# Optimization experiments

Hardware: AMD Instinct MI355X
Metric: run time of the kernel (lower is better)

The kernel has to match this reference:

```python
import jax, jax.numpy as jnp
import numpy as np

B, T, D = 2, 2048, 1024
H, G, K = 16, 4, 64          # num_heads, num_kv_heads, head_dim
R = H // G                   # GQA repeat factor
F = 4096                     # mlp_dim
EPS = 1e-6


def rms_norm(x, scale, eps=EPS):
    var = jnp.mean(x.astype(jnp.float32) ** 2, axis=-1, keepdims=True)
    normed = x * jax.lax.rsqrt(var + eps)
    return (scale * normed).astype(x.dtype)


def apply_rope(x_BTHK, sin_BTK, cos_BTK):
    half = x_BTHK.shape[-1] // 2
    x1, x2 = x_BTHK[..., :half], x_BTHK[..., half:]
    s = sin_BTK[:, :, None, :]
    c = cos_BTK[:, :, None, :]
    return jnp.concatenate([x1 * c - x2 * s, x2 * c + x1 * s], axis=-1).astype(x_BTHK.dtype)


def setup_inputs() -> dict:
    key = jax.random.key(0)
    ks = jax.random.split(key, 12)
    hidden_BTD = jax.random.normal(ks[0], (B, T, D), jnp.float32)
    # rope tables: realistic sin/cos of position*inv_freq
    inv_freq = 1.0 / (10000.0 ** (jnp.arange(K // 2, dtype=jnp.float32) / (K // 2)))
    ang = jnp.arange(T, dtype=jnp.float32)[:, None] * inv_freq[None, :]  # [T, K/2]
    sin_BTK = jnp.broadcast_to(jnp.sin(ang)[None], (B, T, K // 2))
    cos_BTK = jnp.broadcast_to(jnp.cos(ang)[None], (B, T, K // 2))
    mask = jnp.broadcast_to(jnp.tril(jnp.ones((T, T), bool))[None], (B, T, T))
    sc = 1.0 / np.sqrt(D)
    scf = 1.0 / np.sqrt(F)
    return {
        "hidden_BTD": hidden_BTD, "sin_BTK": sin_BTK, "cos_BTK": cos_BTK, "mask": mask,
        "ln1_scale": jnp.ones((D,), jnp.float32),
        "ln2_scale": jnp.ones((D,), jnp.float32),
        "qn_scale": jnp.ones((K,), jnp.float32),
        "kn_scale": jnp.ones((K,), jnp.float32),
        "q_w": jax.random.normal(ks[1], (D, H * K), jnp.float32) * sc,
        "k_w": jax.random.normal(ks[2], (D, G * K), jnp.float32) * sc,
        "v_w": jax.random.normal(ks[3], (D, G * K), jnp.float32) * sc,
        "o_w": jax.random.normal(ks[4], (H * K, D), jnp.float32) * sc,
        "gate_w": jax.random.normal(ks[5], (D, F), jnp.float32) * sc,
        "up_w": jax.random.normal(ks[6], (D, F), jnp.float32) * sc,
        "down_w": jax.random.normal(ks[7], (F, D), jnp.float32) * scf,
    }


def reference(hidden_BTD, sin_BTK, cos_BTK, mask, ln1_scale, ln2_scale,
              qn_scale, kn_scale, q_w, k_w, v_w, o_w, gate_w, up_w, down_w):
    x = rms_norm(hidden_BTD, ln1_scale)
    q = rms_norm((x @ q_w).reshape(B, T, H, K), qn_scale)
    k = rms_norm((x @ k_w).reshape(B, T, G, K), kn_scale)
    v = (x @ v_w).reshape(B, T, G, K)
    q = apply_rope(q, sin_BTK, cos_BTK)
    k = apply_rope(k, sin_BTK, cos_BTK)
    q_BTGRK = q.reshape(B, T, G, R, K)
    scale = K ** (-0.5)
    logits = jnp.einsum('BTGRK,BSGK->BTSGR', q_BTGRK, k) * scale
    neg = float(jnp.finfo(logits.dtype).min)
    logits = jnp.where(mask[:, :, :, None, None], logits, neg)
    weights = jax.nn.softmax(logits.astype(jnp.float32), axis=2).astype(logits.dtype)
    attn = jnp.einsum('BTSGR,BSGK->BTGRK', weights, v).reshape(B, T, H * K)
    hidden_BTD = hidden_BTD + attn @ o_w
    y = rms_norm(hidden_BTD, ln2_scale)
    ff = (jax.nn.silu(y @ gate_w) * (y @ up_w)) @ down_w
    return hidden_BTD + ff
```

## Files before the change

kernel.cpp:

```cpp
#include <hip/hip_runtime.h>
#include <hip/hip_bf16.h>

#define EPSF 1e-6f
constexpr int Bsz  = 2;
constexpr int Tseq = 2048;
constexpr int Dmod = 1024;
constexpr int Hh   = 16;
constexpr int Gg   = 4;
constexpr int Ff   = 4096;
constexpr int Mrows = Bsz * Tseq;

typedef __attribute__((ext_vector_type(8))) short bf16x8;
typedef __attribute__((ext_vector_type(4))) float f32x4;
typedef unsigned short u16;

__device__ inline u16 f2bf(float x) {
    union { float f; unsigned u; } v; v.f = x;
    unsigned r = v.u + 0x7fff + ((v.u >> 16) & 1);
    return (u16)(r >> 16);
}
__device__ inline float bf2f(u16 h) {
    union { unsigned u; float f; } v; v.u = ((unsigned)h) << 16; return v.f;
}

__device__ __forceinline__ void async_copy16(const u16* g, u16* l) {
    __builtin_amdgcn_global_load_lds(
        (const __attribute__((address_space(1))) void*)g,
        (__attribute__((address_space(3))) void*)l, 16, 0, 0);
}


__global__ __launch_bounds__(256) void wprep_all_kernel(
    const float* __restrict__ q_w, const float* __restrict__ k_w,
    const float* __restrict__ v_w, const float* __restrict__ o_w,
    const float* __restrict__ gate_w, const float* __restrict__ up_w,
    const float* __restrict__ down_w,
    u16* __restrict__ QKVT, u16* __restrict__ OTh, u16* __restrict__ OTl,
    u16* __restrict__ GTh, u16* __restrict__ UTh, u16* __restrict__ DTh)
{
    const int bx = blockIdx.x;
    const float* W; u16* Th; u16* Tl = nullptr;
    int N, Kd, ntile, ktile, drow;
    if (bx < 1024) {
        W = q_w; N = 1024; Kd = 1024; ntile = bx & 31; ktile = bx >> 5;
        Th = QKVT; drow = ntile * 32;
    } else if (bx < 1280) {
        const int i = bx - 1024;
        W = k_w; N = 256; Kd = 1024; ntile = i & 7; ktile = i >> 3;
        Th = QKVT; drow = 1024 + ntile * 32;
    } else if (bx < 1536) {
        const int i = bx - 1280;
        W = v_w; N = 256; Kd = 1024; ntile = i & 7; ktile = i >> 3;
        Th = QKVT; drow = 1280 + ntile * 32;
    } else if (bx < 2560) {
        const int i = bx - 1536;
        W = o_w; N = 1024; Kd = 1024; ntile = i & 31; ktile = i >> 5;
        Th = OTh; Tl = OTl; drow = ntile * 32;
    } else if (bx < 6656) {
        const int i = bx - 2560;
        W = gate_w; N = 4096; Kd = 1024; ntile = i & 127; ktile = i >> 7;
        Th = GTh; drow = ntile * 32;
    } else if (bx < 10752) {
        const int i = bx - 6656;
        W = up_w; N = 4096; Kd = 1024; ntile = i & 127; ktile = i >> 7;
        Th = UTh; drow = ntile * 32;
    } else {
        const int i = bx - 10752;
        W = down_w; N = 1024; Kd = 4096; ntile = i & 31; ktile = i >> 5;
        Th = DTh; drow = ntile * 32;
    }
    const int n0 = ntile * 32, k0 = ktile * 32;

    __shared__ float tile[32][33];
    const int r = threadIdx.x >> 3, c4 = (threadIdx.x & 7) * 4;
    const float4 v = *reinterpret_cast<const float4*>(&W[(size_t)(k0 + r) * N + n0 + c4]);
    tile[r][c4 + 0] = v.x; tile[r][c4 + 1] = v.y;
    tile[r][c4 + 2] = v.z; tile[r][c4 + 3] = v.w;
    __syncthreads();
    const int nl = threadIdx.x >> 3, kq = (threadIdx.x & 7) * 4;
    float x0 = tile[kq + 0][nl], x1 = tile[kq + 1][nl];
    float x2 = tile[kq + 2][nl], x3 = tile[kq + 3][nl];
    ushort4 h;
    h.x = f2bf(x0); h.y = f2bf(x1); h.z = f2bf(x2); h.w = f2bf(x3);
    *reinterpret_cast<ushort4*>(&Th[(size_t)(drow + nl) * Kd + k0 + kq]) = h;
    if (Tl) {
        ushort4 l;
        l.x = f2bf(x0 - bf2f(h.x)); l.y = f2bf(x1 - bf2f(h.y));
        l.z = f2bf(x2 - bf2f(h.z)); l.w = f2bf(x3 - bf2f(h.w));
        *reinterpret_cast<ushort4*>(&Tl[(size_t)(drow + nl) * Kd + k0 + kq]) = l;
    }
}

template <int LO>
__global__ __launch_bounds__(256) void rmsnorm_split_kernel(
    const float* __restrict__ x, const float* __restrict__ scale,
    u16* __restrict__ oh, u16* __restrict__ ol)
{
    const int row = blockIdx.x;
    const int tid = threadIdx.x;
    const float4 v = reinterpret_cast<const float4*>(x + (size_t)row * Dmod)[tid];
    float ss = v.x * v.x + v.y * v.y + v.z * v.z + v.w * v.w;
    #pragma unroll
    for (int off = 32; off; off >>= 1) ss += __shfl_xor(ss, off, 64);
    __shared__ float part[4];
    if ((tid & 63) == 0) part[tid >> 6] = ss;
    __syncthreads();
    const float tot = part[0] + part[1] + part[2] + part[3];
    const float rstd = rsqrtf(tot * (1.0f / Dmod) + EPSF);
    const float4 sc = reinterpret_cast<const float4*>(scale)[tid];
    float o0 = v.x * rstd * sc.x, o1 = v.y * rstd * sc.y;
    float o2 = v.z * rstd * sc.z, o3 = v.w * rstd * sc.w;
    ushort4 h;
    h.x = f2bf(o0); h.y = f2bf(o1); h.z = f2bf(o2); h.w = f2bf(o3);
    *reinterpret_cast<ushort4*>(&oh[(size_t)row * Dmod + tid * 4]) = h;
    if (LO) {
        ushort4 l;
        l.x = f2bf(o0 - bf2f(h.x)); l.y = f2bf(o1 - bf2f(h.y));
        l.z = f2bf(o2 - bf2f(h.z)); l.w = f2bf(o3 - bf2f(h.w));
        *reinterpret_cast<ushort4*>(&ol[(size_t)row * Dmod + tid * 4]) = l;
    }
}

template <int ASPLIT, int BSPLIT, int RES>
__global__ __launch_bounds__(256, 2) void mfma_gemm_kernel(
    const u16* __restrict__ Ah, const u16* __restrict__ Al,
    const u16* __restrict__ Bh, const u16* __restrict__ Bl,
    const float* __restrict__ res, float* __restrict__ C,
    int M, int N, int Kd)
{
    __shared__ u16 As_h[128 * 32];
    __shared__ u16 As_l[128 * 32];
    __shared__ u16 Bs_h[128 * 32];
    __shared__ u16 Bs_l[128 * 32];

    const int tid = threadIdx.x;
    const int lane = tid & 63, wave = tid >> 6;
    const int wm = (wave >> 1) * 64, wn = (wave & 1) * 64;
    const int m0 = blockIdx.y * 128, n0 = blockIdx.x * 128;
    const int fm = lane & 15, quad = lane >> 4;
    const int fsw = (fm >> 1) & 3;
    const int fcol = ((quad ^ fsw) * 8);

    f32x4 acc[4][4];
    #pragma unroll
    for (int i = 0; i < 4; ++i)
        #pragma unroll
        for (int j = 0; j < 4; ++j) acc[i][j] = (f32x4){0.f, 0.f, 0.f, 0.f};

    const int lrow = lane >> 2;
    const int lchunk = lane & 3;
    const int schunk = lchunk ^ ((lrow >> 1) & 3);

    for (int k0 = 0; k0 < Kd; k0 += 32) {
        __syncthreads();
        #pragma unroll
        for (int p = 0; p < 2; ++p) {
            const int row = wave * 32 + p * 16 + lrow;
            const size_t ga = (size_t)(m0 + row) * Kd + k0 + schunk * 8;
            const size_t gb = (size_t)(n0 + row) * Kd + k0 + schunk * 8;
            const int ls = row * 32 + lchunk * 8;
            async_copy16(&Ah[ga], &As_h[ls]);
            if (ASPLIT) async_copy16(&Al[ga], &As_l[ls]);
            async_copy16(&Bh[gb], &Bs_h[ls]);
            if (BSPLIT) async_copy16(&Bl[gb], &Bs_l[ls]);
        }
        __syncthreads();

        bf16x8 ah[4], al[4], bh[4], bl[4];
        #pragma unroll
        for (int t = 0; t < 4; ++t) {
            const int ra = (wm + t * 16 + fm) * 32 + fcol;
            const int rb = (wn + t * 16 + fm) * 32 + fcol;
            ah[t] = *reinterpret_cast<const bf16x8*>(&As_h[ra]);
            bh[t] = *reinterpret_cast<const bf16x8*>(&Bs_h[rb]);
            if (ASPLIT) al[t] = *reinterpret_cast<const bf16x8*>(&As_l[ra]);
            if (BSPLIT) bl[t] = *reinterpret_cast<const bf16x8*>(&Bs_l[rb]);
        }
        #pragma unroll
        for (int mt = 0; mt < 4; ++mt)
            #pragma unroll
            for (int nt = 0; nt < 4; ++nt) {
                acc[mt][nt] = __builtin_amdgcn_mfma_f32_16x16x32_bf16(
                    ah[mt], bh[nt], acc[mt][nt], 0, 0, 0);
                if (BSPLIT)
                    acc[mt][nt] = __builtin_amdgcn_mfma_f32_16x16x32_bf16(
                        ah[mt], bl[nt], acc[mt][nt], 0, 0, 0);
                if (ASPLIT)
                    acc[mt][nt] = __builtin_amdgcn_mfma_f32_16x16x32_bf16(
                        al[mt], bh[nt], acc[mt][nt], 0, 0, 0);
            }
    }

    const int cr = (lane >> 4) * 4, cn = lane & 15;
    #pragma unroll
    for (int mt = 0; mt < 4; ++mt)
        #pragma unroll
        for (int nt = 0; nt < 4; ++nt)
            #pragma unroll
            for (int r = 0; r < 4; ++r) {
                const int gm = m0 + wm + mt * 16 + cr + r;
                const int gn = n0 + wn + nt * 16 + cn;
                float v = acc[mt][nt][r];
                if (RES) v += res[(size_t)gm * N + gn];
                C[(size_t)gm * N + gn] = v;
            }
}

__global__ __launch_bounds__(256, 2) void qkv_fused_kernel(
    const u16* __restrict__ Ah, const u16* __restrict__ Bh,
    const float* __restrict__ qn, const float* __restrict__ kn,
    const float* __restrict__ sinp, const float* __restrict__ cosp,
    u16* __restrict__ Qbh, u16* __restrict__ Qbl,
    u16* __restrict__ Kbh, u16* __restrict__ Kbl,
    u16* __restrict__ Vth, u16* __restrict__ Vtl)
{
    __shared__ u16 As_h[128 * 32];
    __shared__ u16 Bs_h[128 * 32];

    const int Kd = 1024;
    const int tid = threadIdx.x;
    const int lane = tid & 63, wave = tid >> 6;
    const int wm = (wave >> 1) * 64, wn = (wave & 1) * 64;
    const int m0 = blockIdx.y * 128, n0 = blockIdx.x * 128;
    const int fm = lane & 15, quad = lane >> 4;
    const int fsw = (fm >> 1) & 3;
    const int fcol = ((quad ^ fsw) * 8);

    f32x4 acc[4][4];
    #pragma unroll
    for (int i = 0; i < 4; ++i)
        #pragma unroll
        for (int j = 0; j < 4; ++j) acc[i][j] = (f32x4){0.f, 0.f, 0.f, 0.f};

    const int lrow = lane >> 2;
    const int lchunk = lane & 3;
    const int schunk = lchunk ^ ((lrow >> 1) & 3);

    for (int k0 = 0; k0 < Kd; k0 += 32) {
        __syncthreads();
        #pragma unroll
        for (int p = 0; p < 2; ++p) {
            const int row = wave * 32 + p * 16 + lrow;
            const size_t ga = (size_t)(m0 + row) * Kd + k0 + schunk * 8;
            const size_t gb = (size_t)(n0 + row) * Kd + k0 + schunk * 8;
            const int ls = row * 32 + lchunk * 8;
            async_copy16(&Ah[ga], &As_h[ls]);
            async_copy16(&Bh[gb], &Bs_h[ls]);
        }
        __syncthreads();

        bf16x8 ah[4], bh[4];
        #pragma unroll
        for (int t = 0; t < 4; ++t) {
            ah[t] = *reinterpret_cast<const bf16x8*>(&As_h[(wm + t * 16 + fm) * 32 + fcol]);
            bh[t] = *reinterpret_cast<const bf16x8*>(&Bs_h[(wn + t * 16 + fm) * 32 + fcol]);
        }
        #pragma unroll
        for (int mt = 0; mt < 4; ++mt)
            #pragma unroll
            for (int nt = 0; nt < 4; ++nt)
                acc[mt][nt] = __builtin_amdgcn_mfma_f32_16x16x32_bf16(
                    ah[mt], bh[nt], acc[mt][nt], 0, 0, 0);
    }

    const int gn0 = n0 + wn;
    const int l15 = lane & 15;

    if (gn0 < 1280) {
        const bool isQ = (gn0 < 1024);
        const float* nsc = isQ ? qn : kn;
        const float osc = isQ ? 0.125f : 1.0f;
        u16* __restrict__ oh = isQ ? Qbh : Kbh;
        u16* __restrict__ ol = isQ ? Qbl : Kbl;
        const int rowstride = isQ ? 1024 : 256;
        const int colbase = isQ ? gn0 : gn0 - 1024;
        float sc[4];
        #pragma unroll
        for (int nt = 0; nt < 4; ++nt) sc[nt] = nsc[nt * 16 + l15];

        #pragma unroll
        for (int mt = 0; mt < 4; ++mt)
            #pragma unroll
            for (int r = 0; r < 4; ++r) {
                const int bt = m0 + wm + mt * 16 + quad * 4 + r;
                float v[4];
                #pragma unroll
                for (int nt = 0; nt < 4; ++nt) v[nt] = acc[mt][nt][r];
                float ss = v[0] * v[0] + v[1] * v[1] + v[2] * v[2] + v[3] * v[3];
                #pragma unroll
                for (int off = 1; off < 16; off <<= 1)
                    ss += __shfl_xor(ss, off, 16);
                const float rstd = rsqrtf(ss * (1.0f / 64.0f) + EPSF);
                float nv[4];
                #pragma unroll
                for (int nt = 0; nt < 4; ++nt) nv[nt] = v[nt] * rstd * sc[nt];
                const float s0 = sinp[bt * 32 + l15];
                const float c0 = cosp[bt * 32 + l15];
                const float s1 = sinp[bt * 32 + 16 + l15];
                const float c1 = cosp[bt * 32 + 16 + l15];
                float o[4];
                o[0] = (nv[0] * c0 - nv[2] * s0) * osc;
                o[1] = (nv[1] * c1 - nv[3] * s1) * osc;
                o[2] = (nv[2] * c0 + nv[0] * s0) * osc;
                o[3] = (nv[3] * c1 + nv[1] * s1) * osc;
                #pragma unroll
                for (int nt = 0; nt < 4; ++nt) {
                    const size_t off = (size_t)bt * rowstride + colbase + nt * 16 + l15;
                    const u16 hi = f2bf(o[nt]);
                    oh[off] = hi;
                    ol[off] = f2bf(o[nt] - bf2f(hi));
                }
            }
    } else {
        const int g = (gn0 - 1280) >> 6;
        const int b = (m0 + wm) >> 11;
        const int tb = ((m0 + wm) & 2047) + quad * 4;
        #pragma unroll
        for (int mt = 0; mt < 4; ++mt)
            #pragma unroll
            for (int nt = 0; nt < 4; ++nt) {
                const float v0 = acc[mt][nt][0], v1 = acc[mt][nt][1];
                const float v2 = acc[mt][nt][2], v3 = acc[mt][nt][3];
                ushort4 hv, lv;
                hv.x = f2bf(v0); hv.y = f2bf(v1); hv.z = f2bf(v2); hv.w = f2bf(v3);
                lv.x = f2bf(v0 - bf2f(hv.x)); lv.y = f2bf(v1 - bf2f(hv.y));
                lv.z = f2bf(v2 - bf2f(hv.z)); lv.w = f2bf(v3 - bf2f(hv.w));
                const size_t off =
                    ((size_t)((b * 4 + g) * 64 + nt * 16 + l15)) * Tseq + tb + mt * 16;
                *reinterpret_cast<ushort4*>(&Vth[off]) = hv;
                *reinterpret_cast<ushort4*>(&Vtl[off]) = lv;
            }
    }
}

#define GU_PHASE_SYNC()                                       \
    __builtin_amdgcn_s_barrier();                             \
    asm volatile("s_waitcnt lgkmcnt(0)" ::: "memory");        \
    __builtin_amdgcn_sched_barrier(0)

#define GU_MFMA4(MBASE, AF)                                                      \
    _Pragma("unroll")                                                            \
    for (int mf = 0; mf < 4; ++mf) {                                             \
        accg[(MBASE) + mf][0] = __builtin_amdgcn_mfma_f32_16x16x32_bf16(         \
            AF[mf], bgf[0], accg[(MBASE) + mf][0], 0, 0, 0);                     \
        accu[(MBASE) + mf][0] = __builtin_amdgcn_mfma_f32_16x16x32_bf16(         \
            AF[mf], buf2[0], accu[(MBASE) + mf][0], 0, 0, 0);                    \
        accg[(MBASE) + mf][1] = __builtin_amdgcn_mfma_f32_16x16x32_bf16(         \
            AF[mf], bgf[1], accg[(MBASE) + mf][1], 0, 0, 0);                     \
        accu[(MBASE) + mf][1] = __builtin_amdgcn_mfma_f32_16x16x32_bf16(         \
            AF[mf], buf2[1], accu[(MBASE) + mf][1], 0, 0, 0);                    \
    }

__global__ __launch_bounds__(512, 2) void gateup8_kernel(
    const u16* __restrict__ Yh, const u16* __restrict__ Yl,
    const u16* __restrict__ Gw, const u16* __restrict__ Uw,
    u16* __restrict__ FF)
{
    constexpr int NK = 32;
    __shared__ u16 AsH[3][256 * 32];
    __shared__ u16 AsL[3][256 * 32];
    __shared__ u16 Gs[3][128 * 32];
    __shared__ u16 Us[3][128 * 32];

    const int tid  = threadIdx.x;
    const int lane = tid & 63;
    const int wave = tid >> 6;
    const int wave_m = wave >> 2;
    const int wave_n = wave & 3;

    const int wg  = blockIdx.x;
    const int xcd = wg & 7;
    const int idx = wg >> 3;
    const int ntile = xcd * 4 + (idx & 3);
    const int mtile = idx >> 2;
    const int m0 = mtile * 256, n0 = ntile * 128;

    const int fm = lane & 15, quad = lane >> 4;
    const int fsw = (fm >> 1) & 3;
    const int fcol = (quad ^ fsw) * 8;

    f32x4 accg[8][2], accu[8][2];
    #pragma unroll
    for (int i = 0; i < 8; ++i)
        #pragma unroll
        for (int j = 0; j < 2; ++j) {
            accg[i][j] = (f32x4){0.f, 0.f, 0.f, 0.f};
            accu[i][j] = (f32x4){0.f, 0.f, 0.f, 0.f};
        }

    const int srow = tid >> 2;
    const int schk = tid & 3;
    const int sw   = schk ^ ((srow >> 1) & 3);
    const u16* aSrc0 = &Yh[(size_t)(m0 + srow) * 1024 + sw * 8];
    const u16* aSrc1 = &Yh[(size_t)(m0 + srow + 128) * 1024 + sw * 8];
    const u16* lSrc0 = &Yl[(size_t)(m0 + srow) * 1024 + sw * 8];
    const u16* lSrc1 = &Yl[(size_t)(m0 + srow + 128) * 1024 + sw * 8];
    const u16* gSrc  = &Gw[(size_t)(n0 + srow) * 1024 + sw * 8];
    const u16* uSrc  = &Uw[(size_t)(n0 + srow) * 1024 + sw * 8];
    const int aDst0 = srow * 32 + schk * 8;
    const int aDst1 = aDst0 + 128 * 32;

#define STAGE_AH(T, BUF) do {                                  \
        async_copy16(aSrc0 + (T) * 32, &AsH[BUF][aDst0]);      \
        async_copy16(aSrc1 + (T) * 32, &AsH[BUF][aDst1]); } while (0)
#define STAGE_AL(T, BUF) do {                                  \
        async_copy16(lSrc0 + (T) * 32, &AsL[BUF][aDst0]);      \
        async_copy16(lSrc1 + (T) * 32, &AsL[BUF][aDst1]); } while (0)
#define STAGE_B(T, BUF) do {                                   \
        async_copy16(gSrc + (T) * 32, &Gs[BUF][aDst0]);        \
        async_copy16(uSrc + (T) * 32, &Us[BUF][aDst0]); } while (0)

    int raOff[8], rbOff[2];
    #pragma unroll
    for (int mf = 0; mf < 8; ++mf)
        raOff[mf] = (wave_m * 128 + mf * 16 + fm) * 32 + fcol;
    #pragma unroll
    for (int nf = 0; nf < 2; ++nf)
        rbOff[nf] = (wave_n * 32 + nf * 16 + fm) * 32 + fcol;

    STAGE_AH(0, 0); STAGE_AL(0, 0); STAGE_B(0, 0);
    STAGE_AH(1, 1); STAGE_AL(1, 1); STAGE_B(1, 1);
    asm volatile("s_waitcnt vmcnt(6)" ::: "memory");
    __builtin_amdgcn_s_barrier();

    int bcur = 0, bnxt = 2;
    #pragma unroll 1
    for (int t = 0; t < NK; ++t) {
        const bool pf = (t + 2 < NK);
        bf16x8 bgf[2], buf2[2];

        {
            #pragma unroll
            for (int nf = 0; nf < 2; ++nf) {
                bgf[nf]  = *reinterpret_cast<const bf16x8*>(&Gs[bcur][rbOff[nf]]);
                buf2[nf] = *reinterpret_cast<const bf16x8*>(&Us[bcur][rbOff[nf]]);
            }
            bf16x8 af[4];
            #pragma unroll
            for (int mf = 0; mf < 4; ++mf)
                af[mf] = *reinterpret_cast<const bf16x8*>(&AsH[bcur][raOff[mf]]);
            if (pf) STAGE_AH(t + 2, bnxt);
            GU_PHASE_SYNC();
            __builtin_amdgcn_s_setprio(1);
            GU_MFMA4(0, af);
            __builtin_amdgcn_s_setprio(0);
            __builtin_amdgcn_s_barrier();
        }
        {
            bf16x8 af[4];
            #pragma unroll
            for (int mf = 0; mf < 4; ++mf)
                af[mf] = *reinterpret_cast<const bf16x8*>(&AsH[bcur][raOff[mf + 4]]);
            if (pf) STAGE_AL(t + 2, bnxt);
            GU_PHASE_SYNC();
            __builtin_amdgcn_s_setprio(1);
            GU_MFMA4(4, af);
            __builtin_amdgcn_s_setprio(0);
            __builtin_amdgcn_s_barrier();
        }
        {
            bf16x8 af[4];
            #pragma unroll
            for (int mf = 0; mf < 4; ++mf)
                af[mf] = *reinterpret_cast<const bf16x8*>(&AsL[bcur][raOff[mf]]);
            if (pf) STAGE_B(t + 2, bnxt);
            GU_PHASE_SYNC();
            __builtin_amdgcn_s_setprio(1);
            GU_MFMA4(0, af);
            __builtin_amdgcn_s_setprio(0);
            __builtin_amdgcn_s_barrier();
        }
        {
            bf16x8 af[4];
            #pragma unroll
            for (int mf = 0; mf < 4; ++mf)
                af[mf] = *reinterpret_cast<const bf16x8*>(&AsL[bcur][raOff[mf + 4]]);
            GU_PHASE_SYNC();
            __builtin_amdgcn_s_setprio(1);
            GU_MFMA4(4, af);
            __builtin_amdgcn_s_setprio(0);
            if (t + 2 < NK) {
                asm volatile("s_waitcnt vmcnt(6)" ::: "memory");
            } else if (t + 1 < NK) {
                asm volatile("s_waitcnt vmcnt(0)" ::: "memory");
            }
            __builtin_amdgcn_s_barrier();
        }

        bcur = (bcur == 2) ? 0 : bcur + 1;
        bnxt = (bnxt == 2) ? 0 : bnxt + 1;
    }
#undef STAGE_AH
#undef STAGE_AL
#undef STAGE_B

    const int cr = quad * 4;
    #pragma unroll
    for (int mf = 0; mf < 8; ++mf)
        #pragma unroll
        for (int nf = 0; nf < 2; ++nf)
            #pragma unroll
            for (int r = 0; r < 4; ++r) {
                const int gm = m0 + wave_m * 128 + mf * 16 + cr + r;
                const int gn = n0 + wave_n * 32 + nf * 16 + fm;
                const float g = accg[mf][nf][r];
                const float ff = (g / (1.0f + __expf(-g))) * accu[mf][nf][r];
                FF[(size_t)gm * Ff + gn] = f2bf(ff);
            }
}

__global__ __launch_bounds__(256) void attn_mfma_kernel(
    const u16* __restrict__ Qh, const u16* __restrict__ Ql,
    const u16* __restrict__ Kh, const u16* __restrict__ Kl,
    const u16* __restrict__ Vth, const u16* __restrict__ Vtl,
    u16* __restrict__ AOh, u16* __restrict__ AOl)
{
    __shared__ u16 KsH[64 * 72];
    __shared__ u16 KsL[64 * 72];
    __shared__ u16 VsH[64 * 72];
    __shared__ u16 VsL[64 * 72];
    __shared__ u16 Ps[4][16 * 72];

    const int tid = threadIdx.x;
    const int wave = tid >> 6, lane = tid & 63;
    const int l15 = lane & 15, quad = lane >> 4;

    const int bg = blockIdx.x & 7;
    const int b = bg >> 2, g = bg & 3;
    const int win = 127 - (blockIdx.x >> 3);
    const int t0 = win * 16;
    const int h = g * 4 + wave;

    bf16x8 qh[2], ql[2];
    {
        const size_t qrow = (size_t)(b * Tseq + t0 + l15) * 1024 + h * 64;
        #pragma unroll
        for (int ks = 0; ks < 2; ++ks) {
            qh[ks] = *reinterpret_cast<const bf16x8*>(&Qh[qrow + ks * 32 + quad * 8]);
            ql[ks] = *reinterpret_cast<const bf16x8*>(&Ql[qrow + ks * 32 + quad * 8]);
        }
    }

    const int srow = tid >> 2;
    const int scol = (tid & 3) * 16;
    const size_t kgb = (size_t)(b * Tseq) * 256 + g * 64 + scol;
    const size_t vgb = (size_t)(bg * 64 + srow) * Tseq + scol;

    const int nit = t0 / 64 + 1;

    uint4 ck0, ck1, cl0, cl1, cv0, cv1, cw0, cw1;
    {
        const size_t ka = kgb + (size_t)srow * 256;
        ck0 = *reinterpret_cast<const uint4*>(&Kh[ka]);
        ck1 = *reinterpret_cast<const uint4*>(&Kh[ka + 8]);
        cl0 = *reinterpret_cast<const uint4*>(&Kl[ka]);
        cl1 = *reinterpret_cast<const uint4*>(&Kl[ka + 8]);
        cv0 = *reinterpret_cast<const uint4*>(&Vth[vgb]);
        cv1 = *reinterpret_cast<const uint4*>(&Vth[vgb + 8]);
        cw0 = *reinterpret_cast<const uint4*>(&Vtl[vgb]);
        cw1 = *reinterpret_cast<const uint4*>(&Vtl[vgb + 8]);
    }

    f32x4 oacc[4];
    #pragma unroll
    for (int nt = 0; nt < 4; ++nt) oacc[nt] = (f32x4){0.f, 0.f, 0.f, 0.f};
    float m_r[4], l_r[4];
    #pragma unroll
    for (int r = 0; r < 4; ++r) { m_r[r] = -1e30f; l_r[r] = 0.0f; }

    u16* psw = &Ps[wave][0];
    const int lb = srow * 72 + scol;

    for (int it = 0; it < nit; ++it) {
        const int s0 = it * 64;
        const bool diag = (it == nit - 1);

        __syncthreads();
        *reinterpret_cast<uint4*>(&KsH[lb])     = ck0;
        *reinterpret_cast<uint4*>(&KsH[lb + 8]) = ck1;
        *reinterpret_cast<uint4*>(&KsL[lb])     = cl0;
        *reinterpret_cast<uint4*>(&KsL[lb + 8]) = cl1;
        *reinterpret_cast<uint4*>(&VsH[lb])     = cv0;
        *reinterpret_cast<uint4*>(&VsH[lb + 8]) = cv1;
        *reinterpret_cast<uint4*>(&VsL[lb])     = cw0;
        *reinterpret_cast<uint4*>(&VsL[lb + 8]) = cw1;
        if (it + 1 < nit) {
            const size_t ka = kgb + (size_t)(s0 + 64 + srow) * 256;
            ck0 = *reinterpret_cast<const uint4*>(&Kh[ka]);
            ck1 = *reinterpret_cast<const uint4*>(&Kh[ka + 8]);
            cl0 = *reinterpret_cast<const uint4*>(&Kl[ka]);
            cl1 = *reinterpret_cast<const uint4*>(&Kl[ka + 8]);
            const size_t va = vgb + s0 + 64;
            cv0 = *reinterpret_cast<const uint4*>(&Vth[va]);
            cv1 = *reinterpret_cast<const uint4*>(&Vth[va + 8]);
            cw0 = *reinterpret_cast<const uint4*>(&Vtl[va]);
            cw1 = *reinterpret_cast<const uint4*>(&Vtl[va + 8]);
        }
        __syncthreads();

        f32x4 sacc[4];
        #pragma unroll
        for (int nt = 0; nt < 4; ++nt) sacc[nt] = (f32x4){0.f, 0.f, 0.f, 0.f};

        #pragma unroll
        for (int ks = 0; ks < 2; ++ks) {
            bf16x8 kfh[4], kfl[4];
            #pragma unroll
            for (int nt = 0; nt < 4; ++nt) {
                const int a = (nt * 16 + l15) * 72 + ks * 32 + quad * 8;
                kfh[nt] = *reinterpret_cast<const bf16x8*>(&KsH[a]);
                kfl[nt] = *reinterpret_cast<const bf16x8*>(&KsL[a]);
            }
            #pragma unroll
            for (int nt = 0; nt < 4; ++nt) {
                sacc[nt] = __builtin_amdgcn_mfma_f32_16x16x32_bf16(qh[ks], kfh[nt], sacc[nt], 0, 0, 0);
                sacc[nt] = __builtin_amdgcn_mfma_f32_16x16x32_bf16(ql[ks], kfh[nt], sacc[nt], 0, 0, 0);
                sacc[nt] = __builtin_amdgcn_mfma_f32_16x16x32_bf16(qh[ks], kfl[nt], sacc[nt], 0, 0, 0);
            }
        }

        if (diag) {
            #pragma unroll
            for (int nt = 0; nt < 4; ++nt) {
                const int sg = s0 + nt * 16 + l15;
                #pragma unroll
                for (int r = 0; r < 4; ++r)
                    if (sg > t0 + quad * 4 + r) sacc[nt][r] = -1e30f;
            }
        }

        #pragma unroll
        for (int r = 0; r < 4; ++r) {
            float mx = fmaxf(fmaxf(sacc[0][r], sacc[1][r]),
                             fmaxf(sacc[2][r], sacc[3][r]));
            #pragma unroll
            for (int off = 1; off < 16; off <<= 1)
                mx = fmaxf(mx, __shfl_xor(mx, off, 16));
            const float mnew = fmaxf(m_r[r], mx);
            const float alpha = __expf(m_r[r] - mnew);
            m_r[r] = mnew;

            float rs = 0.0f;
            #pragma unroll
            for (int nt = 0; nt < 4; ++nt) {
                const float p = __expf(sacc[nt][r] - mnew);
                sacc[nt][r] = p;
                rs += p;
            }
            #pragma unroll
            for (int off = 1; off < 16; off <<= 1)
                rs += __shfl_xor(rs, off, 16);
            l_r[r] = l_r[r] * alpha + rs;
            #pragma unroll
            for (int nt = 0; nt < 4; ++nt) oacc[nt][r] *= alpha;
            #pragma unroll
            for (int nt = 0; nt < 4; ++nt)
                psw[(quad * 4 + r) * 72 + nt * 16 + l15] = f2bf(sacc[nt][r]);
        }

        #pragma unroll
        for (int ks = 0; ks < 2; ++ks) {
            const bf16x8 pa = *reinterpret_cast<const bf16x8*>(
                &psw[l15 * 72 + ks * 32 + quad * 8]);
            bf16x8 vfh[4], vfl[4];
            #pragma unroll
            for (int nt = 0; nt < 4; ++nt) {
                const int a = (nt * 16 + l15) * 72 + ks * 32 + quad * 8;
                vfh[nt] = *reinterpret_cast<const bf16x8*>(&VsH[a]);
                vfl[nt] = *reinterpret_cast<const bf16x8*>(&VsL[a]);
            }
            #pragma unroll
            for (int nt = 0; nt < 4; ++nt) {
                oacc[nt] = __builtin_amdgcn_mfma_f32_16x16x32_bf16(pa, vfh[nt], oacc[nt], 0, 0, 0);
                oacc[nt] = __builtin_amdgcn_mfma_f32_16x16x32_bf16(pa, vfl[nt], oacc[nt], 0, 0, 0);
            }
        }
    }

    #pragma unroll
    for (int r = 0; r < 4; ++r) {
        const float inv = 1.0f / l_r[r];
        const size_t orow = (size_t)(b * Tseq + t0 + quad * 4 + r) * 1024 + h * 64;
        #pragma unroll
        for (int nt = 0; nt < 4; ++nt) {
            const float o = oacc[nt][r] * inv;
            const u16 hi = f2bf(o);
            AOh[orow + nt * 16 + l15] = hi;
            AOl[orow + nt * 16 + l15] = f2bf(o - bf2f(hi));
        }
    }
}

extern "C" void kernel_launch(void* const* d_in, const int* in_sizes, int n_in,
                              void* d_out, int out_size, void* d_ws,
                              size_t ws_size, hipStream_t stream)
{
    const float* hidden = (const float*)d_in[0];
    const float* sinp   = (const float*)d_in[1];
    const float* cosp   = (const float*)d_in[2];
    const float* ln1    = (const float*)d_in[4];
    const float* ln2    = (const float*)d_in[5];
    const float* qn     = (const float*)d_in[6];
    const float* kn     = (const float*)d_in[7];
    const float* q_w    = (const float*)d_in[8];
    const float* k_w    = (const float*)d_in[9];
    const float* v_w    = (const float*)d_in[10];
    const float* o_w    = (const float*)d_in[11];
    const float* gate_w = (const float*)d_in[12];
    const float* up_w   = (const float*)d_in[13];
    const float* down_w = (const float*)d_in[14];
    float* out = (float*)d_out;

    char* base = (char*)d_ws;
    u16*   OTh  = (u16*)(base);
    u16*   OTl  = (u16*)(base + 2097152);
    u16*   GTh  = (u16*)(base + 4194304);
    u16*   UTh  = (u16*)(base + 12582912);
    u16*   DTh  = (u16*)(base + 20971520);
    u16*   QKVT = (u16*)(base + 29360128);
    u16*   Xh   = (u16*)(base + 32505856);
    u16*   Qbh  = (u16*)(base + 40894464);
    u16*   Qbl  = (u16*)(base + 49283072);
    u16*   Kbh  = (u16*)(base + 57671680);
    u16*   Kbl  = (u16*)(base + 59768832);
    u16*   Vth  = (u16*)(base + 61865984);
    u16*   Vtl  = (u16*)(base + 63963136);
    u16*   AOh  = (u16*)(base + 66060288);
    u16*   AOl  = (u16*)(base + 74448896);
    u16*   FFh  = (u16*)(base + 82837504);

    float* H2 = (float*)Qbh;
    u16*   Yh = Kbh;
    u16*   Yl = AOh;

    wprep_all_kernel<<<14848, 256, 0, stream>>>(
        q_w, k_w, v_w, o_w, gate_w, up_w, down_w,
        QKVT, OTh, OTl, GTh, UTh, DTh);

    rmsnorm_split_kernel<0><<<Mrows, 256, 0, stream>>>(hidden, ln1, Xh, nullptr);

    qkv_fused_kernel<<<dim3(12, 32), 256, 0, stream>>>(
        Xh, QKVT, qn, kn, sinp, cosp, Qbh, Qbl, Kbh, Kbl, Vth, Vtl);

    attn_mfma_kernel<<<Bsz * Gg * (Tseq / 16), 256, 0, stream>>>(
        Qbh, Qbl, Kbh, Kbl, Vth, Vtl, AOh, AOl);

    mfma_gemm_kernel<1, 1, 1><<<dim3(8, 32), 256, 0, stream>>>(
        AOh, AOl, OTh, OTl, hidden, H2, Mrows, Dmod, 1024);

    rmsnorm_split_kernel<1><<<Mrows, 256, 0, stream>>>(H2, ln2, Yh, Yl);

    gateup8_kernel<<<512, 512, 0, stream>>>(Yh, Yl, GTh, UTh, FFh);

    mfma_gemm_kernel<0, 0, 1><<<dim3(8, 32), 256, 0, stream>>>(
        FFh, nullptr, DTh, nullptr, H2, out, Mrows, Dmod, 4096);
}
```

Baseline: 521.5 us.

## Switch gate/up GEMM to 32x32x16 MFMA with two-phase pipeline and manual unroll

Rewrites the gate/up FFN kernel to use 32x32x16 bf16 MFMA tiles instead of 16x16x32, which cuts LDS fragment reads per FLOP and the number of MFMA issues. The four per-iteration phases become two (hi and lo activation halves), so there are fewer barriers per K-step. The triple-buffer rotation is unrolled by three with constant buffer indices, and the epilogue is remapped to the 32x32 accumulator layout. This adds register pressure and a different LDS swizzle access pattern, and prefetches are grouped more densely in the second phase.

```diff
diff --git a/kernel.cpp b/kernel.cpp
--- a/kernel.cpp
+++ b/kernel.cpp
@@ -12,6 +12,7 @@
 
 typedef __attribute__((ext_vector_type(8))) short bf16x8;
 typedef __attribute__((ext_vector_type(4))) float f32x4;
+typedef __attribute__((ext_vector_type(16))) float f32x16;
 typedef unsigned short u16;
 
 __device__ inline u16 f2bf(float x) {
@@ -338,20 +339,7 @@
     asm volatile("s_waitcnt lgkmcnt(0)" ::: "memory");        \
     __builtin_amdgcn_sched_barrier(0)
 
-#define GU_MFMA4(MBASE, AF)                                                      \
-    _Pragma("unroll")                                                            \
-    for (int mf = 0; mf < 4; ++mf) {                                             \
-        accg[(MBASE) + mf][0] = __builtin_amdgcn_mfma_f32_16x16x32_bf16(         \
-            AF[mf], bgf[0], accg[(MBASE) + mf][0], 0, 0, 0);                     \
-        accu[(MBASE) + mf][0] = __builtin_amdgcn_mfma_f32_16x16x32_bf16(         \
-            AF[mf], buf2[0], accu[(MBASE) + mf][0], 0, 0, 0);                    \
-        accg[(MBASE) + mf][1] = __builtin_amdgcn_mfma_f32_16x16x32_bf16(         \
-            AF[mf], bgf[1], accg[(MBASE) + mf][1], 0, 0, 0);                     \
-        accu[(MBASE) + mf][1] = __builtin_amdgcn_mfma_f32_16x16x32_bf16(         \
-            AF[mf], buf2[1], accu[(MBASE) + mf][1], 0, 0, 0);                    \
-    }
-
-__global__ __launch_bounds__(512, 2) void gateup8_kernel(
+__global__ __launch_bounds__(512, 2) void gateup32_kernel(
     const u16* __restrict__ Yh, const u16* __restrict__ Yl,
     const u16* __restrict__ Gw, const u16* __restrict__ Uw,
     u16* __restrict__ FF)
@@ -375,18 +363,15 @@
     const int mtile = idx >> 2;
     const int m0 = mtile * 256, n0 = ntile * 128;
 
-    const int fm = lane & 15, quad = lane >> 4;
-    const int fsw = (fm >> 1) & 3;
-    const int fcol = (quad ^ fsw) * 8;
-
-    f32x4 accg[8][2], accu[8][2];
-    #pragma unroll
-    for (int i = 0; i < 8; ++i)
-        #pragma unroll
-        for (int j = 0; j < 2; ++j) {
-            accg[i][j] = (f32x4){0.f, 0.f, 0.f, 0.f};
-            accu[i][j] = (f32x4){0.f, 0.f, 0.f, 0.f};
-        }
+    const int l31 = lane & 31;
+    const int khi = lane >> 5;
+
+    f32x16 accg[4], accu[4];
+    #pragma unroll
+    for (int i = 0; i < 4; ++i) {
+        accg[i] = (f32x16)(0.f);
+        accu[i] = (f32x16)(0.f);
+    }
 
     const int srow = tid >> 2;
     const int schk = tid & 3;
@@ -410,103 +395,110 @@
         async_copy16(gSrc + (T) * 32, &Gs[BUF][aDst0]);        \
         async_copy16(uSrc + (T) * 32, &Us[BUF][aDst0]); } while (0)
 
-    int raOff[8], rbOff[2];
-    #pragma unroll
-    for (int mf = 0; mf < 8; ++mf)
-        raOff[mf] = (wave_m * 128 + mf * 16 + fm) * 32 + fcol;
-    #pragma unroll
-    for (int nf = 0; nf < 2; ++nf)
-        rbOff[nf] = (wave_n * 32 + nf * 16 + fm) * 32 + fcol;
+    int aOff[4][2], bOff[2];
+    #pragma unroll
+    for (int mf = 0; mf < 4; ++mf)
+        #pragma unroll
+        for (int h = 0; h < 2; ++h) {
+            const int ra = wave_m * 128 + mf * 32 + l31;
+            aOff[mf][h] = ra * 32 + (((2 * h + khi) ^ ((ra >> 1) & 3)) * 8);
+        }
+    #pragma unroll
+    for (int h = 0; h < 2; ++h) {
+        const int rb = wave_n * 32 + l31;
+        bOff[h] = rb * 32 + (((2 * h + khi) ^ ((rb >> 1) & 3)) * 8);
+    }
+
+#define GU_STEP(BC, BN, T, PF, GATE) do {                                       \
+    bf16x8 bg[2], bu[2];                                                        \
+    {                                                    \
+        bf16x8 ah[4][2];                                                        \
+        _Pragma("unroll")                                                       \
+        for (int h = 0; h < 2; ++h) {                                           \
+            bg[h] = *reinterpret_cast<const bf16x8*>(&Gs[BC][bOff[h]]);         \
+            bu[h] = *reinterpret_cast<const bf16x8*>(&Us[BC][bOff[h]]);         \
+        }                                                                       \
+        _Pragma("unroll")                                                       \
+        for (int mf = 0; mf < 4; ++mf)                                          \
+            _Pragma("unroll")                                                   \
+            for (int h = 0; h < 2; ++h)                                         \
+                ah[mf][h] = *reinterpret_cast<const bf16x8*>(                   \
+                    &AsH[BC][aOff[mf][h]]);                                     \
+        if (PF) STAGE_AH((T) + 2, BN);                                          \
+        GU_PHASE_SYNC();                                                        \
+        __builtin_amdgcn_s_setprio(1);                                          \
+        _Pragma("unroll")                                                       \
+        for (int mf = 0; mf < 4; ++mf)                                          \
+            _Pragma("unroll")                                                   \
+            for (int h = 0; h < 2; ++h) {                                       \
+                accg[mf] = __builtin_amdgcn_mfma_f32_32x32x16_bf16(             \
+                    ah[mf][h], bg[h], accg[mf], 0, 0, 0);                       \
+                accu[mf] = __builtin_amdgcn_mfma_f32_32x32x16_bf16(             \
+                    ah[mf][h], bu[h], accu[mf], 0, 0, 0);                       \
+            }                                                                   \
+        __builtin_amdgcn_s_setprio(0);                                          \
+        __builtin_amdgcn_s_barrier();                                           \
+    }                                                                           \
+    {                                                    \
+        bf16x8 al[4][2];                                                        \
+        _Pragma("unroll")                                                       \
+        for (int mf = 0; mf < 4; ++mf)                                          \
+            _Pragma("unroll")                                                   \
+            for (int h = 0; h < 2; ++h)                                         \
+                al[mf][h] = *reinterpret_cast<const bf16x8*>(                   \
+                    &AsL[BC][aOff[mf][h]]);                                     \
+        if (PF) { STAGE_AL((T) + 2, BN); STAGE_B((T) + 2, BN); }                \
+        GU_PHASE_SYNC();                                                        \
+        __builtin_amdgcn_s_setprio(1);                                          \
+        _Pragma("unroll")                                                       \
+        for (int mf = 0; mf < 4; ++mf)                                          \
+            _Pragma("unroll")                                                   \
+            for (int h = 0; h < 2; ++h) {                                       \
+                accg[mf] = __builtin_amdgcn_mfma_f32_32x32x16_bf16(             \
+                    al[mf][h], bg[h], accg[mf], 0, 0, 0);                       \
+                accu[mf] = __builtin_amdgcn_mfma_f32_32x32x16_bf16(             \
+                    al[mf][h], bu[h], accu[mf], 0, 0, 0);                       \
+            }                                                                   \
+        __builtin_amdgcn_s_setprio(0);                                          \
+        if ((GATE) == 6) {                                                      \
+            asm volatile("s_waitcnt vmcnt(6)" ::: "memory");                    \
+        } else if ((GATE) == 0) {                                               \
+            asm volatile("s_waitcnt vmcnt(0)" ::: "memory");                    \
+        }                                                                       \
+        __builtin_amdgcn_s_barrier();                                           \
+    }                                                                           \
+} while (0)
 
     STAGE_AH(0, 0); STAGE_AL(0, 0); STAGE_B(0, 0);
     STAGE_AH(1, 1); STAGE_AL(1, 1); STAGE_B(1, 1);
     asm volatile("s_waitcnt vmcnt(6)" ::: "memory");
     __builtin_amdgcn_s_barrier();
 
-    int bcur = 0, bnxt = 2;
     #pragma unroll 1
-    for (int t = 0; t < NK; ++t) {
-        const bool pf = (t + 2 < NK);
-        bf16x8 bgf[2], buf2[2];
-
-        {
-            #pragma unroll
-            for (int nf = 0; nf < 2; ++nf) {
-                bgf[nf]  = *reinterpret_cast<const bf16x8*>(&Gs[bcur][rbOff[nf]]);
-                buf2[nf] = *reinterpret_cast<const bf16x8*>(&Us[bcur][rbOff[nf]]);
-            }
-            bf16x8 af[4];
-            #pragma unroll
-            for (int mf = 0; mf < 4; ++mf)
-                af[mf] = *reinterpret_cast<const bf16x8*>(&AsH[bcur][raOff[mf]]);
-            if (pf) STAGE_AH(t + 2, bnxt);
-            GU_PHASE_SYNC();
-            __builtin_amdgcn_s_setprio(1);
-            GU_MFMA4(0, af);
-            __builtin_amdgcn_s_setprio(0);
-            __builtin_amdgcn_s_barrier();
-        }
-        {
-            bf16x8 af[4];
-            #pragma unroll
-            for (int mf = 0; mf < 4; ++mf)
-                af[mf] = *reinterpret_cast<const bf16x8*>(&AsH[bcur][raOff[mf + 4]]);
-            if (pf) STAGE_AL(t + 2, bnxt);
-            GU_PHASE_SYNC();
-            __builtin_amdgcn_s_setprio(1);
-            GU_MFMA4(4, af);
-            __builtin_amdgcn_s_setprio(0);
-            __builtin_amdgcn_s_barrier();
-        }
-        {
-            bf16x8 af[4];
-            #pragma unroll
-            for (int mf = 0; mf < 4; ++mf)
-                af[mf] = *reinterpret_cast<const bf16x8*>(&AsL[bcur][raOff[mf]]);
-            if (pf) STAGE_B(t + 2, bnxt);
-            GU_PHASE_SYNC();
-            __builtin_amdgcn_s_setprio(1);
-            GU_MFMA4(0, af);
-            __builtin_amdgcn_s_setprio(0);
-            __builtin_amdgcn_s_barrier();
-        }
-        {
-            bf16x8 af[4];
-            #pragma unroll
-            for (int mf = 0; mf < 4; ++mf)
-                af[mf] = *reinterpret_cast<const bf16x8*>(&AsL[bcur][raOff[mf + 4]]);
-            GU_PHASE_SYNC();
-            __builtin_amdgcn_s_setprio(1);
-            GU_MFMA4(4, af);
-            __builtin_amdgcn_s_setprio(0);
-            if (t + 2 < NK) {
-                asm volatile("s_waitcnt vmcnt(6)" ::: "memory");
-            } else if (t + 1 < NK) {
-                asm volatile("s_waitcnt vmcnt(0)" ::: "memory");
-            }
-            __builtin_amdgcn_s_barrier();
-        }
-
-        bcur = (bcur == 2) ? 0 : bcur + 1;
-        bnxt = (bnxt == 2) ? 0 : bnxt + 1;
-    }
+    for (int t3 = 0; t3 < NK - 2; t3 += 3) {
+        GU_STEP(0, 2, t3 + 0, true, 6);
+        GU_STEP(1, 0, t3 + 1, true, 6);
+        GU_STEP(2, 1, t3 + 2, true, 6);
+    }
+    GU_STEP(0, 2, 30, false, 0);
+    GU_STEP(1, 0, 31, false, -1);
+
+#undef GU_STEP
 #undef STAGE_AH
 #undef STAGE_AL
 #undef STAGE_B
 
-    const int cr = quad * 4;
-    #pragma unroll
-    for (int mf = 0; mf < 8; ++mf)
-        #pragma unroll
-        for (int nf = 0; nf < 2; ++nf)
-            #pragma unroll
-            for (int r = 0; r < 4; ++r) {
-                const int gm = m0 + wave_m * 128 + mf * 16 + cr + r;
-                const int gn = n0 + wave_n * 32 + nf * 16 + fm;
-                const float g = accg[mf][nf][r];
-                const float ff = (g / (1.0f + __expf(-g))) * accu[mf][nf][r];
-                FF[(size_t)gm * Ff + gn] = f2bf(ff);
-            }
+    #pragma unroll
+    for (int mf = 0; mf < 4; ++mf)
+        #pragma unroll
+        for (int reg = 0; reg < 16; ++reg) {
+            const int crow = (reg & 3) + 8 * (reg >> 2) + 4 * khi;
+            const int gm = m0 + wave_m * 128 + mf * 32 + crow;
+            const int gn = n0 + wave_n * 32 + l31;
+            const float g = accg[mf][reg];
+            const float ff = (g / (1.0f + __expf(-g))) * accu[mf][reg];
+            FF[(size_t)gm * Ff + gn] = f2bf(ff);
+        }
 }
 
 __global__ __launch_bounds__(256) void attn_mfma_kernel(
@@ -750,7 +742,7 @@
 
     rmsnorm_split_kernel<1><<<Mrows, 256, 0, stream>>>(H2, ln2, Yh, Yl);
 
-    gateup8_kernel<<<512, 512, 0, stream>>>(Yh, Yl, GTh, UTh, FFh);
+    gateup32_kernel<<<512, 512, 0, stream>>>(Yh, Yl, GTh, UTh, FFh);
 
     mfma_gemm_kernel<0, 0, 1><<<dim3(8, 32), 256, 0, stream>>>(
         FFh, nullptr, DTh, nullptr, H2, out, Mrows, Dmod, 4096);
```

Result: slower. 534.3 us (+2.5%).

## Triple-buffer async loads in output GEMMs with explicit vmcnt gating

Applied to the files above, without the earlier changes.

Replaces the single-buffered GEMM used for the output projection and down projection with a three-stage software pipeline. Global-to-LDS async copies are issued two k-steps ahead and gated by explicit vmcnt waits, with raised wave priority around the MFMA block. The aim is to hide load latency and drop one barrier per k-step. It triples LDS use per block, which may lower occupancy for the split-precision variant, and it fixes K at compile time.

```diff
diff --git a/kernel.cpp b/kernel.cpp
--- a/kernel.cpp
+++ b/kernel.cpp
@@ -121,17 +121,21 @@
     }
 }
 
-template <int ASPLIT, int BSPLIT, int RES>
-__global__ __launch_bounds__(256, 2) void mfma_gemm_kernel(
+template <int NKT, int ASPLIT, int BSPLIT, int RES>
+__global__ __launch_bounds__(256, 2) void mfma_gemm_pipe(
     const u16* __restrict__ Ah, const u16* __restrict__ Al,
     const u16* __restrict__ Bh, const u16* __restrict__ Bl,
     const float* __restrict__ res, float* __restrict__ C,
-    int M, int N, int Kd)
+    int M, int N)
 {
-    __shared__ u16 As_h[128 * 32];
-    __shared__ u16 As_l[128 * 32];
-    __shared__ u16 Bs_h[128 * 32];
-    __shared__ u16 Bs_l[128 * 32];
+    constexpr int Kd = NKT * 32;
+    constexpr int NI = 4 + 4 * ASPLIT * 0 + 2 * ASPLIT + 2 * BSPLIT;
+    static_assert((NKT - 2) % 3 == 0, "main loop unroll-3");
+
+    __shared__ u16 AsH[3][128 * 32];
+    __shared__ u16 BsH[3][128 * 32];
+    __shared__ u16 AsL[ASPLIT ? 3 : 1][128 * 32];
+    __shared__ u16 BsL[BSPLIT ? 3 : 1][128 * 32];
 
     const int tid = threadIdx.x;
     const int lane = tid & 63, wave = tid >> 6;
@@ -139,7 +143,7 @@
     const int m0 = blockIdx.y * 128, n0 = blockIdx.x * 128;
     const int fm = lane & 15, quad = lane >> 4;
     const int fsw = (fm >> 1) & 3;
-    const int fcol = ((quad ^ fsw) * 8);
+    const int fcol = (quad ^ fsw) * 8;
 
     f32x4 acc[4][4];
     #pragma unroll
@@ -147,49 +151,97 @@
         #pragma unroll
         for (int j = 0; j < 4; ++j) acc[i][j] = (f32x4){0.f, 0.f, 0.f, 0.f};
 
-    const int lrow = lane >> 2;
-    const int lchunk = lane & 3;
-    const int schunk = lchunk ^ ((lrow >> 1) & 3);
-
-    for (int k0 = 0; k0 < Kd; k0 += 32) {
-        __syncthreads();
-        #pragma unroll
-        for (int p = 0; p < 2; ++p) {
-            const int row = wave * 32 + p * 16 + lrow;
-            const size_t ga = (size_t)(m0 + row) * Kd + k0 + schunk * 8;
-            const size_t gb = (size_t)(n0 + row) * Kd + k0 + schunk * 8;
-            const int ls = row * 32 + lchunk * 8;
-            async_copy16(&Ah[ga], &As_h[ls]);
-            if (ASPLIT) async_copy16(&Al[ga], &As_l[ls]);
-            async_copy16(&Bh[gb], &Bs_h[ls]);
-            if (BSPLIT) async_copy16(&Bl[gb], &Bs_l[ls]);
-        }
-        __syncthreads();
-
-        bf16x8 ah[4], al[4], bh[4], bl[4];
-        #pragma unroll
-        for (int t = 0; t < 4; ++t) {
-            const int ra = (wm + t * 16 + fm) * 32 + fcol;
-            const int rb = (wn + t * 16 + fm) * 32 + fcol;
-            ah[t] = *reinterpret_cast<const bf16x8*>(&As_h[ra]);
-            bh[t] = *reinterpret_cast<const bf16x8*>(&Bs_h[rb]);
-            if (ASPLIT) al[t] = *reinterpret_cast<const bf16x8*>(&As_l[ra]);
-            if (BSPLIT) bl[t] = *reinterpret_cast<const bf16x8*>(&Bs_l[rb]);
-        }
-        #pragma unroll
-        for (int mt = 0; mt < 4; ++mt)
-            #pragma unroll
-            for (int nt = 0; nt < 4; ++nt) {
-                acc[mt][nt] = __builtin_amdgcn_mfma_f32_16x16x32_bf16(
-                    ah[mt], bh[nt], acc[mt][nt], 0, 0, 0);
-                if (BSPLIT)
-                    acc[mt][nt] = __builtin_amdgcn_mfma_f32_16x16x32_bf16(
-                        ah[mt], bl[nt], acc[mt][nt], 0, 0, 0);
-                if (ASPLIT)
-                    acc[mt][nt] = __builtin_amdgcn_mfma_f32_16x16x32_bf16(
-                        al[mt], bh[nt], acc[mt][nt], 0, 0, 0);
-            }
-    }
+    const int srow = tid >> 2;
+    const int schk = tid & 3;
+    const int sw   = schk ^ ((srow >> 1) & 3);
+    const u16* aS0 = &Ah[(size_t)(m0 + srow) * Kd + sw * 8];
+    const u16* aS1 = &Ah[(size_t)(m0 + srow + 64) * Kd + sw * 8];
+    const u16* bS0 = &Bh[(size_t)(n0 + srow) * Kd + sw * 8];
+    const u16* bS1 = &Bh[(size_t)(n0 + srow + 64) * Kd + sw * 8];
+    const u16* alS0 = ASPLIT ? &Al[(size_t)(m0 + srow) * Kd + sw * 8] : nullptr;
+    const u16* alS1 = ASPLIT ? &Al[(size_t)(m0 + srow + 64) * Kd + sw * 8] : nullptr;
+    const u16* blS0 = BSPLIT ? &Bl[(size_t)(n0 + srow) * Kd + sw * 8] : nullptr;
+    const u16* blS1 = BSPLIT ? &Bl[(size_t)(n0 + srow + 64) * Kd + sw * 8] : nullptr;
+    const int dst0 = srow * 32 + schk * 8;
+    const int dst1 = dst0 + 64 * 32;
+
+#define PSTAGE(T, BUF) do {                                                  \
+        async_copy16(aS0 + (T) * 32, &AsH[BUF][dst0]);                       \
+        async_copy16(aS1 + (T) * 32, &AsH[BUF][dst1]);                       \
+        if (ASPLIT) {                                                        \
+            async_copy16(alS0 + (T) * 32, &AsL[BUF][dst0]);                  \
+            async_copy16(alS1 + (T) * 32, &AsL[BUF][dst1]);                  \
+        }                                                                    \
+        async_copy16(bS0 + (T) * 32, &BsH[BUF][dst0]);                       \
+        async_copy16(bS1 + (T) * 32, &BsH[BUF][dst1]);                       \
+        if (BSPLIT) {                                                        \
+            async_copy16(blS0 + (T) * 32, &BsL[BUF][dst0]);                  \
+            async_copy16(blS1 + (T) * 32, &BsL[BUF][dst1]);                  \
+        }                                                                    \
+    } while (0)
+
+#define PGATE(GATE) do {                                                     \
+        if ((GATE) == 1) {                                                   \
+            if constexpr (NI == 4)                                           \
+                asm volatile("s_waitcnt vmcnt(4)" ::: "memory");             \
+            else                                                             \
+                asm volatile("s_waitcnt vmcnt(8)" ::: "memory");             \
+        } else if ((GATE) == 0) {                                            \
+            asm volatile("s_waitcnt vmcnt(0)" ::: "memory");                 \
+        }                                                                    \
+    } while (0)
+
+#define PSTEP(BC, BN, T, PF, GATE) do {                                      \
+    bf16x8 ah[4], bh[4], al[4], bl[4];                                       \
+    _Pragma("unroll")                                                        \
+    for (int t = 0; t < 4; ++t) {                                            \
+        const int ra = (wm + t * 16 + fm) * 32 + fcol;                       \
+        const int rb = (wn + t * 16 + fm) * 32 + fcol;                       \
+        ah[t] = *reinterpret_cast<const bf16x8*>(&AsH[BC][ra]);              \
+        bh[t] = *reinterpret_cast<const bf16x8*>(&BsH[BC][rb]);              \
+        if (ASPLIT) al[t] = *reinterpret_cast<const bf16x8*>(&AsL[BC][ra]);  \
+        if (BSPLIT) bl[t] = *reinterpret_cast<const bf16x8*>(&BsL[BC][rb]);  \
+    }                                                                        \
+    if (PF) PSTAGE((T) + 2, BN);                                             \
+    __builtin_amdgcn_s_barrier();                                            \
+    asm volatile("s_waitcnt lgkmcnt(0)" ::: "memory");                       \
+    __builtin_amdgcn_sched_barrier(0);                                       \
+    __builtin_amdgcn_s_setprio(1);                                           \
+    _Pragma("unroll")                                                        \
+    for (int mt = 0; mt < 4; ++mt)                                           \
+        _Pragma("unroll")                                                    \
+        for (int nt = 0; nt < 4; ++nt) {                                     \
+            acc[mt][nt] = __builtin_amdgcn_mfma_f32_16x16x32_bf16(           \
+                ah[mt], bh[nt], acc[mt][nt], 0, 0, 0);                       \
+            if (BSPLIT)                                                      \
+                acc[mt][nt] = __builtin_amdgcn_mfma_f32_16x16x32_bf16(       \
+                    ah[mt], bl[nt], acc[mt][nt], 0, 0, 0);                   \
+            if (ASPLIT)                                                      \
+                acc[mt][nt] = __builtin_amdgcn_mfma_f32_16x16x32_bf16(       \
+                    al[mt], bh[nt], acc[mt][nt], 0, 0, 0);                   \
+        }                                                                    \
+    __builtin_amdgcn_s_setprio(0);                                           \
+    PGATE(GATE);                                                             \
+    __builtin_amdgcn_s_barrier();                                            \
+} while (0)
+
+    PSTAGE(0, 0);
+    PSTAGE(1, 1);
+    PGATE(1);
+    __builtin_amdgcn_s_barrier();
+
+    #pragma unroll 1
+    for (int t3 = 0; t3 < NKT - 2; t3 += 3) {
+        PSTEP(0, 2, t3 + 0, true, 1);
+        PSTEP(1, 0, t3 + 1, true, 1);
+        PSTEP(2, 1, t3 + 2, true, 1);
+    }
+    PSTEP(0, 2, NKT - 2, false, 0);
+    PSTEP(1, 0, NKT - 1, false, -1);
+
+#undef PSTEP
+#undef PGATE
+#undef PSTAGE
 
     const int cr = (lane >> 4) * 4, cn = lane & 15;
     #pragma unroll
@@ -745,13 +797,13 @@
     attn_mfma_kernel<<<Bsz * Gg * (Tseq / 16), 256, 0, stream>>>(
         Qbh, Qbl, Kbh, Kbl, Vth, Vtl, AOh, AOl);
 
-    mfma_gemm_kernel<1, 1, 1><<<dim3(8, 32), 256, 0, stream>>>(
-        AOh, AOl, OTh, OTl, hidden, H2, Mrows, Dmod, 1024);
+    mfma_gemm_pipe<32, 1, 1, 1><<<dim3(8, 32), 256, 0, stream>>>(
+        AOh, AOl, OTh, OTl, hidden, H2, Mrows, Dmod);
 
     rmsnorm_split_kernel<1><<<Mrows, 256, 0, stream>>>(H2, ln2, Yh, Yl);
 
     gateup8_kernel<<<512, 512, 0, stream>>>(Yh, Yl, GTh, UTh, FFh);
 
-    mfma_gemm_kernel<0, 0, 1><<<dim3(8, 32), 256, 0, stream>>>(
-        FFh, nullptr, DTh, nullptr, H2, out, Mrows, Dmod, 4096);
-}
+    mfma_gemm_pipe<128, 0, 0, 1><<<dim3(8, 32), 256, 0, stream>>>(
+        FFh, nullptr, DTh, nullptr, H2, out, Mrows, Dmod);
+}
```

New measurement: 498.9 us. 1.05x faster.
